# Kernel tuning notes

Measured on AMD Instinct MI355X. Metric: run time of the kernel, lower is better.

The kernel has to match this reference:

```python
import jax, jax.numpy as jnp
import numpy as np

N_NODES = 50000
N_EDGES = 800000
D_IN = 128
D_OUT = 128


def setup_inputs() -> dict:
    key = jax.random.key(0)
    k1, k2, k3, k4, k5 = jax.random.split(key, 5)
    x = jax.random.normal(k1, (N_NODES, D_IN), dtype=jnp.float32)
    # fc weight, torch Linear convention: [out_dim, in_dim]
    W = jax.random.normal(k2, (D_OUT, D_IN), dtype=jnp.float32) * (1.0 / np.sqrt(D_IN))
    # attn_fc weight: [1, 2*out_dim], no bias
    a = jax.random.normal(k3, (1, 2 * D_OUT), dtype=jnp.float32) * (1.0 / np.sqrt(2 * D_OUT))
    src = jax.random.randint(k4, (N_EDGES,), 0, N_NODES)
    dst = jax.random.randint(k5, (N_EDGES,), 0, N_NODES)
    return {"x": x, "W": W, "a": a, "src": src, "dst": dst}


def reference(x, W, a, src, dst):
    # h = fc(x)
    h = x @ W.T  # [N, D_OUT]
    # attn_fc(cat([h_src, h_dst])) == h_src @ a[:D] + h_dst @ a[D:] (linear, no bias),
    # so precompute per-node scalars instead of materializing [E, 2*D_OUT].
    a_src = a[0, :D_OUT]
    a_dst = a[0, D_OUT:]
    s = h @ a_src  # [N]
    d = h @ a_dst  # [N]
    e = jax.nn.sigmoid(s[src] + d[dst])[:, None]  # [E, 1]
    msg = e * h[src]  # [E, D_OUT]  edge gather + weight
    # reduce: f[v] = sum over incoming edges of e * h_src
    f = jax.ops.segment_sum(msg, dst, num_segments=N_NODES)  # [N, D_OUT]
    return f
```

## Files before the change

### kernel.cpp

```cpp
#include <hip/hip_runtime.h>
#include <hip/hip_bf16.h>
#include <stdint.h>

#define NN 50000
#define NE 800000
#define DD 128
#define NBKT 1563
#define BCH 4096
#define BGRID ((NE + BCH - 1) / BCH)
#define CAP 640
#define SPILL_CAP 32768
#define GROWS 64
#define GGRID ((NN + GROWS - 1) / GROWS)

typedef __attribute__((ext_vector_type(8))) unsigned short ushort8;
typedef __attribute__((ext_vector_type(8))) short short8;
typedef __attribute__((ext_vector_type(4))) float f32x4;

__device__ inline uint32_t cvtpk(float lo, float hi) {
    uint32_t r;
    asm("v_cvt_pk_bf16_f32 %0, %1, %2" : "=v"(r) : "v"(lo), "v"(hi));
    return r;
}
__device__ inline float bf_lo(uint32_t u) { return __uint_as_float(u << 16); }
__device__ inline float bf_hi(uint32_t u) { return __uint_as_float(u & 0xffff0000u); }

__global__ __launch_bounds__(256) void prep_k(const float* __restrict__ W,
                                              uint16_t* __restrict__ Wb,
                                              int* __restrict__ cntg) {
    int t = threadIdx.x;
    if (blockIdx.x == 0) {
        for (int k = t; k < NBKT + 4; k += 256) cntg[k] = 0;
    }
    int i = blockIdx.x * 256 + t;
    if (i < DD * DD) {
        uint32_t u = __float_as_uint(W[i]);
        Wb[i] = (uint16_t)((u + 0x7fffu + ((u >> 16) & 1u)) >> 16);
    }
}

__global__ __launch_bounds__(256) void fused_k(const float* __restrict__ x,
                                               const uint16_t* __restrict__ Wb,
                                               const float* __restrict__ a,
                                               const int* __restrict__ src,
                                               const int* __restrict__ dst,
                                               uint16_t* __restrict__ hb,
                                               float* __restrict__ sArr,
                                               float* __restrict__ dArr,
                                               int* __restrict__ cntg,
                                               int* __restrict__ scnt,
                                               uint32_t* __restrict__ rec,
                                               uint2* __restrict__ spill) {
    __shared__ int lh[NBKT];
    __shared__ int gb[NBKT];
    const int t = threadIdx.x;

    if ((int)blockIdx.x < GGRID) {
        const int l = t & 63, wid = t >> 6;
        const int r0 = blockIdx.x * GROWS;
        const int lr = l & 15, lk = l >> 4;

        f32x4 acc[8];
        #pragma unroll
        for (int c = 0; c < 8; ++c) acc[c] = f32x4{0.f, 0.f, 0.f, 0.f};

        const int arow = r0 + wid * 16 + lr;
        const int lrow = (arow < NN) ? arow : (NN - 1);
        const float* xp = x + (size_t)lrow * DD + lk * 8;

        #pragma unroll
        for (int kc = 0; kc < 4; ++kc) {
            float4 v0 = *(const float4*)(xp + kc * 32);
            float4 v1 = *(const float4*)(xp + kc * 32 + 4);
            union { uint32_t u[4]; short8 s; } A;
            A.u[0] = cvtpk(v0.x, v0.y); A.u[1] = cvtpk(v0.z, v0.w);
            A.u[2] = cvtpk(v1.x, v1.y); A.u[3] = cvtpk(v1.z, v1.w);
            #pragma unroll
            for (int c = 0; c < 8; ++c) {
                int col = c * 16 + lr;
                short8 bf_ = *(const short8*)(Wb + (size_t)col * DD + kc * 32 + lk * 8);
                acc[c] = __builtin_amdgcn_mfma_f32_16x16x32_bf16(A.s, bf_, acc[c], 0, 0, 0);
            }
        }

        float avs[8], avd[8];
        #pragma unroll
        for (int c = 0; c < 8; ++c) {
            avs[c] = a[c * 16 + lr];
            avd[c] = a[DD + c * 16 + lr];
        }
        #pragma unroll
        for (int i = 0; i < 4; ++i) {
            float ps = 0.f, pd = 0.f;
            #pragma unroll
            for (int c = 0; c < 8; ++c) {
                ps = fmaf(acc[c][i], avs[c], ps);
                pd = fmaf(acc[c][i], avd[c], pd);
            }
            #pragma unroll
            for (int o = 8; o > 0; o >>= 1) {
                ps += __shfl_xor(ps, o);
                pd += __shfl_xor(pd, o);
            }
            int row = r0 + wid * 16 + lk * 4 + i;
            if (lr == 0 && row < NN) { sArr[row] = ps; dArr[row] = pd; }
        }

        #pragma unroll
        for (int i = 0; i < 4; ++i) {
            int row = r0 + wid * 16 + lk * 4 + i;
            if (row < NN) {
                union { uint32_t u[4]; ushort8 s; } H;
                H.u[0] = cvtpk(acc[0][i], acc[1][i]);
                H.u[1] = cvtpk(acc[2][i], acc[3][i]);
                H.u[2] = cvtpk(acc[4][i], acc[5][i]);
                H.u[3] = cvtpk(acc[6][i], acc[7][i]);
                *(ushort8*)(hb + (size_t)row * DD + lr * 8) = H.s;
            }
        }
    } else {
        int bb = blockIdx.x - GGRID;
        for (int k = t; k < NBKT; k += 256) lh[k] = 0;
        __syncthreads();
        int base = bb * BCH;
        unsigned pk[16]; int bk[16];
        #pragma unroll
        for (int i = 0; i < 16; ++i) {
            int idx = base + i * 256 + t;
            if (idx < NE) {
                int s_ = src[idx], d_ = dst[idx];
                bk[i] = d_ >> 5;
                pk[i] = ((unsigned)(d_ & 31) << 16) | (unsigned)s_;
                atomicAdd(&lh[bk[i]], 1);
            } else bk[i] = -1;
        }
        __syncthreads();
        for (int k = t; k < NBKT; k += 256) {
            int c = lh[k];
            lh[k] = 0;
            gb[k] = c ? atomicAdd(&cntg[k], c) : 0;
        }
        __syncthreads();
        #pragma unroll
        for (int i = 0; i < 16; ++i) {
            if (bk[i] >= 0) {
                int sl = atomicAdd(&lh[bk[i]], 1);
                int p = gb[bk[i]] + sl;
                if (p < CAP) {
                    rec[(size_t)bk[i] * CAP + p] = pk[i];
                } else {
                    int sp = atomicAdd(scnt, 1);
                    if (sp < SPILL_CAP)
                        spill[sp] = make_uint2(pk[i] & 0xffffu,
                                               (unsigned)(bk[i] * 32 + (int)(pk[i] >> 16)));
                }
            }
        }
    }
}

__global__ __launch_bounds__(256) void bsort_agg_k(const uint16_t* __restrict__ hb,
                                                   const float* __restrict__ sA,
                                                   const float* __restrict__ dA,
                                                   const int* __restrict__ cntg,
                                                   const uint32_t* __restrict__ rec,
                                                   const int* __restrict__ scnt,
                                                   const uint2* __restrict__ spill,
                                                   float* __restrict__ out) {
    __shared__ uint32_t srt[CAP];
    __shared__ float    eL[CAP];
    __shared__ float dAl[32];
    __shared__ int h32[32];
    __shared__ int s33[33];
    __shared__ int curw[32];
    int t = threadIdx.x, l = t & 63, wid = t >> 6;
    int b = blockIdx.x;
    int cnt = cntg[b]; if (cnt > CAP) cnt = CAP;
    int beg = b * CAP;
    int n0 = b * 32;
    int ns = *scnt; if (ns > SPILL_CAP) ns = SPILL_CAP;
    if (t < 32) {
        h32[t] = 0;
        int n = n0 + t;
        dAl[t] = (n < NN) ? dA[n] : 0.f;
    }
    __syncthreads();

    uint32_t rc[3]; float er[3]; int nrc = 0;
    for (int j = t; j < cnt; j += 256) {
        uint32_t r = rec[beg + j];
        rc[nrc] = r;
        atomicAdd(&h32[r >> 16], 1);
        float z = sA[r & 0xffffu] + dAl[r >> 16];
        er[nrc] = 1.f / (1.f + __expf(-z));
        ++nrc;
    }
    __syncthreads();
    if (wid == 0) {
        int v = (l < 32) ? h32[l] : 0;
        int inc = v;
        #pragma unroll
        for (int o = 1; o < 32; o <<= 1) {
            int nb = __shfl_up(inc, o);
            if (l >= o) inc += nb;
        }
        if (l < 32) { s33[l + 1] = inc; curw[l] = inc - v; }
        if (l == 0) s33[0] = 0;
    }
    __syncthreads();
    for (int k = 0; k < nrc; ++k) {
        uint32_t r = rc[k];
        int p = atomicAdd(&curw[r >> 16], 1);
        srt[p] = r;
        eL[p] = er[k];
    }
    __syncthreads();

    const int q = l >> 4, sl = l & 15;
    const char* hbp = (const char*)hb;
    #pragma unroll 1
    for (int rr = 0; rr < 8; ++rr) {
        int d = wid * 8 + rr;
        int n = n0 + d;
        if (n >= NN) break;
        int js = s33[d], je = s33[d + 1];
        float acc[8] = {0.f,0.f,0.f,0.f,0.f,0.f,0.f,0.f};
        for (int j = js; j < je; j += 8) {
            int j0 = j + q, j1 = j + 4 + q;
            bool v0 = j0 < je, v1 = j1 < je;
            uint32_t r0 = srt[v0 ? j0 : js];
            uint32_t r1 = srt[v1 ? j1 : js];
            float e0 = v0 ? eL[j0] : 0.f;
            float e1 = v1 ? eL[j1] : 0.f;
            uint4 u0 = *(const uint4*)(hbp + (size_t)(r0 & 0xffffu) * 256 + sl * 16);
            uint4 u1 = *(const uint4*)(hbp + (size_t)(r1 & 0xffffu) * 256 + sl * 16);
            acc[0] = fmaf(e0, bf_lo(u0.x), acc[0]); acc[1] = fmaf(e0, bf_hi(u0.x), acc[1]);
            acc[2] = fmaf(e0, bf_lo(u0.y), acc[2]); acc[3] = fmaf(e0, bf_hi(u0.y), acc[3]);
            acc[4] = fmaf(e0, bf_lo(u0.z), acc[4]); acc[5] = fmaf(e0, bf_hi(u0.z), acc[5]);
            acc[6] = fmaf(e0, bf_lo(u0.w), acc[6]); acc[7] = fmaf(e0, bf_hi(u0.w), acc[7]);
            acc[0] = fmaf(e1, bf_lo(u1.x), acc[0]); acc[1] = fmaf(e1, bf_hi(u1.x), acc[1]);
            acc[2] = fmaf(e1, bf_lo(u1.y), acc[2]); acc[3] = fmaf(e1, bf_hi(u1.y), acc[3]);
            acc[4] = fmaf(e1, bf_lo(u1.z), acc[4]); acc[5] = fmaf(e1, bf_hi(u1.z), acc[5]);
            acc[6] = fmaf(e1, bf_lo(u1.w), acc[6]); acc[7] = fmaf(e1, bf_hi(u1.w), acc[7]);
        }
        #pragma unroll
        for (int k = 0; k < 8; ++k) {
            acc[k] += __shfl_xor(acc[k], 16);
            acc[k] += __shfl_xor(acc[k], 32);
        }
        if (ns > 0) {
            for (int i = 0; i < ns; ++i) {
                uint2 sp = spill[i];
                if ((int)sp.y == n) {
                    float z = sA[sp.x] + dAl[d];
                    float e = 1.f / (1.f + __expf(-z));
                    uint4 u = *(const uint4*)(hbp + (size_t)sp.x * 256 + sl * 16);
                    acc[0] = fmaf(e, bf_lo(u.x), acc[0]); acc[1] = fmaf(e, bf_hi(u.x), acc[1]);
                    acc[2] = fmaf(e, bf_lo(u.y), acc[2]); acc[3] = fmaf(e, bf_hi(u.y), acc[3]);
                    acc[4] = fmaf(e, bf_lo(u.z), acc[4]); acc[5] = fmaf(e, bf_hi(u.z), acc[5]);
                    acc[6] = fmaf(e, bf_lo(u.w), acc[6]); acc[7] = fmaf(e, bf_hi(u.w), acc[7]);
                }
            }
        }
        float vx = (q == 0) ? acc[0] : (q == 1) ? acc[2] : (q == 2) ? acc[4] : acc[6];
        float vy = (q == 0) ? acc[1] : (q == 1) ? acc[3] : (q == 2) ? acc[5] : acc[7];
        float* orow = out + (size_t)n * DD;
        orow[(2 * q) * 16 + sl]     = vx;
        orow[(2 * q + 1) * 16 + sl] = vy;
    }
}

__global__ __launch_bounds__(256) void edge_atomic_k(const int* __restrict__ src, const int* __restrict__ dst,
                                                     const float* __restrict__ sArr, const float* __restrict__ dArr,
                                                     const uint32_t* __restrict__ hb, float* __restrict__ out) {
    int wid = threadIdx.x >> 6, l = threadIdx.x & 63;
    int e = blockIdx.x * 4 + wid;
    if (e >= NE) return;
    int sv = src[e], dv = dst[e];
    float z = sArr[sv] + dArr[dv];
    float ev = 1.0f / (1.0f + __expf(-z));
    uint32_t u = hb[(size_t)sv * 64 + l];
    int colx = 32 * (l & 3) + (l >> 2);
    atomicAdd(&out[(size_t)dv * DD + colx],      ev * bf_lo(u));
    atomicAdd(&out[(size_t)dv * DD + colx + 16], ev * bf_hi(u));
}

extern "C" void kernel_launch(void* const* d_in, const int* in_sizes, int n_in,
                              void* d_out, int out_size, void* d_ws, size_t ws_size,
                              hipStream_t stream) {
    const float* x  = (const float*)d_in[0];
    const float* W  = (const float*)d_in[1];
    const float* a  = (const float*)d_in[2];
    const int* src  = (const int*)d_in[3];
    const int* dst  = (const int*)d_in[4];
    float* out = (float*)d_out;

    char* p = (char*)d_ws;
    uint16_t* hb = (uint16_t*)p;            p += (size_t)NN * DD * 2;
    uint16_t* Wb = (uint16_t*)p;            p += (size_t)DD * DD * 2;
    float* sA    = (float*)p;               p += (size_t)NN * 4;
    float* dA    = (float*)p;               p += (size_t)NN * 4;
    int*   cntg  = (int*)p;                 p += (size_t)NBKT * 4;
    int*   scnt  = (int*)p;                 p += 16;
    uint32_t* rec = (uint32_t*)(((uintptr_t)p + 15) & ~(uintptr_t)15);
    p = (char*)(rec + (size_t)NBKT * CAP);
    uint2* spill = (uint2*)p;               p += (size_t)SPILL_CAP * 8;
    size_t need  = (size_t)(p - (char*)d_ws);

    if (ws_size >= need) {
        prep_k<<<64, 256, 0, stream>>>(W, Wb, cntg);
        fused_k<<<GGRID + BGRID, 256, 0, stream>>>(x, Wb, a, src, dst,
                                                   hb, sA, dA, cntg, scnt, rec, spill);
        bsort_agg_k<<<NBKT, 256, 0, stream>>>(hb, sA, dA, cntg, rec, scnt, spill, out);
    } else {
        hipMemsetAsync(out, 0, sizeof(float) * (size_t)NN * DD, stream);
        prep_k<<<64, 256, 0, stream>>>(W, Wb, cntg);
        fused_k<<<GGRID, 256, 0, stream>>>(x, Wb, a, src, dst,
                                           hb, sA, dA, cntg, scnt, rec, spill);
        edge_atomic_k<<<NE / 4, 256, 0, stream>>>(src, dst, sA, dA, (const uint32_t*)hb, out);
    }
}
```

Before: 71.34 us.

## Shrink dst buckets to 16 nodes and sort edges by source segment

Halves the destination bucket size (3125 buckets of 16 nodes, CAP 384) so twice as many aggregation blocks run, with less LDS per block. Within each block, edges are binned by destination node and also by a coarse source-node segment (four ranges), and blocks start at staggered segments. The aim is better L2 locality on gathered h rows and more parallelism. Each 16-lane quarter-wave now owns one destination node and walks its edges two at a time, so the cross-quarter shuffle reduction is gone, at the cost of less memory-level parallelism per node and a higher chance of spills with the smaller CAP.

```diff
diff --git a/kernel.cpp b/kernel.cpp
--- a/kernel.cpp
+++ b/kernel.cpp
@@ -5,13 +5,14 @@
 #define NN 50000
 #define NE 800000
 #define DD 128
-#define NBKT 1563
+#define NBKT 3125
 #define BCH 4096
 #define BGRID ((NE + BCH - 1) / BCH)
-#define CAP 640
+#define CAP 384
 #define SPILL_CAP 32768
 #define GROWS 64
 #define GGRID ((NN + GROWS - 1) / GROWS)
+#define NSEG 4
 
 typedef __attribute__((ext_vector_type(8))) unsigned short ushort8;
 typedef __attribute__((ext_vector_type(8))) short short8;
@@ -29,8 +30,8 @@
                                               uint16_t* __restrict__ Wb,
                                               int* __restrict__ cntg) {
     int t = threadIdx.x;
-    if (blockIdx.x == 0) {
-        for (int k = t; k < NBKT + 4; k += 256) cntg[k] = 0;
+    if (blockIdx.x < 13) {
+        for (int k = blockIdx.x * 256 + t; k < NBKT + 4; k += 13 * 256) cntg[k] = 0;
     }
     int i = blockIdx.x * 256 + t;
     if (i < DD * DD) {
@@ -129,8 +130,8 @@
             int idx = base + i * 256 + t;
             if (idx < NE) {
                 int s_ = src[idx], d_ = dst[idx];
-                bk[i] = d_ >> 5;
-                pk[i] = ((unsigned)(d_ & 31) << 16) | (unsigned)s_;
+                bk[i] = d_ >> 4;
+                pk[i] = ((unsigned)(d_ & 15) << 16) | (unsigned)s_;
                 atomicAdd(&lh[bk[i]], 1);
             } else bk[i] = -1;
         }
@@ -152,7 +153,7 @@
                     int sp = atomicAdd(scnt, 1);
                     if (sp < SPILL_CAP)
                         spill[sp] = make_uint2(pk[i] & 0xffffu,
-                                               (unsigned)(bk[i] * 32 + (int)(pk[i] >> 16)));
+                                               (unsigned)(bk[i] * 16 + (int)(pk[i] >> 16)));
                 }
             }
         }
@@ -169,68 +170,71 @@
                                                    float* __restrict__ out) {
     __shared__ uint32_t srt[CAP];
     __shared__ float    eL[CAP];
-    __shared__ float dAl[32];
-    __shared__ int h32[32];
-    __shared__ int s33[33];
-    __shared__ int curw[32];
+    __shared__ float dAl[16];
+    __shared__ int hbin[NSEG * 16];
+    __shared__ int soff[NSEG * 16 + 1];
+    __shared__ int curw[NSEG * 16];
     int t = threadIdx.x, l = t & 63, wid = t >> 6;
     int b = blockIdx.x;
     int cnt = cntg[b]; if (cnt > CAP) cnt = CAP;
     int beg = b * CAP;
-    int n0 = b * 32;
+    int n0 = b * 16;
     int ns = *scnt; if (ns > SPILL_CAP) ns = SPILL_CAP;
-    if (t < 32) {
-        h32[t] = 0;
-        int n = n0 + t;
-        dAl[t] = (n < NN) ? dA[n] : 0.f;
-    }
+    if (t < 64) hbin[t] = 0;
+    if (t < 16) dAl[t] = dA[n0 + t];
     __syncthreads();
 
-    uint32_t rc[3]; float er[3]; int nrc = 0;
+    uint32_t rc[2]; float er[2]; int bn[2]; int nrc = 0;
     for (int j = t; j < cnt; j += 256) {
         uint32_t r = rec[beg + j];
-        rc[nrc] = r;
-        atomicAdd(&h32[r >> 16], 1);
-        float z = sA[r & 0xffffu] + dAl[r >> 16];
+        int sv = (int)(r & 0xffffu);
+        int sg = (sv >= 12500) + (sv >= 25000) + (sv >= 37500);
+        int bin = (sg << 4) | (int)(r >> 16);
+        rc[nrc] = r; bn[nrc] = bin;
+        atomicAdd(&hbin[bin], 1);
+        float z = sA[sv] + dAl[r >> 16];
         er[nrc] = 1.f / (1.f + __expf(-z));
         ++nrc;
     }
     __syncthreads();
     if (wid == 0) {
-        int v = (l < 32) ? h32[l] : 0;
+        int v = hbin[l];
         int inc = v;
         #pragma unroll
-        for (int o = 1; o < 32; o <<= 1) {
+        for (int o = 1; o < 64; o <<= 1) {
             int nb = __shfl_up(inc, o);
             if (l >= o) inc += nb;
         }
-        if (l < 32) { s33[l + 1] = inc; curw[l] = inc - v; }
-        if (l == 0) s33[0] = 0;
+        soff[l + 1] = inc;
+        if (l == 0) soff[0] = 0;
+        curw[l] = inc - v;
     }
     __syncthreads();
     for (int k = 0; k < nrc; ++k) {
-        uint32_t r = rc[k];
-        int p = atomicAdd(&curw[r >> 16], 1);
-        srt[p] = r;
+        int p = atomicAdd(&curw[bn[k]], 1);
+        srt[p] = rc[k];
         eL[p] = er[k];
     }
     __syncthreads();
 
     const int q = l >> 4, sl = l & 15;
+    const int d = wid * 4 + q;
+    const int n = n0 + d;
     const char* hbp = (const char*)hb;
-    #pragma unroll 1
-    for (int rr = 0; rr < 8; ++rr) {
-        int d = wid * 8 + rr;
-        int n = n0 + d;
-        if (n >= NN) break;
-        int js = s33[d], je = s33[d + 1];
-        float acc[8] = {0.f,0.f,0.f,0.f,0.f,0.f,0.f,0.f};
-        for (int j = js; j < je; j += 8) {
-            int j0 = j + q, j1 = j + 4 + q;
-            bool v0 = j0 < je, v1 = j1 < je;
-            uint32_t r0 = srt[v0 ? j0 : js];
-            uint32_t r1 = srt[v1 ? j1 : js];
-            float e0 = v0 ? eL[j0] : 0.f;
+    const int s0 = (blockIdx.x & 7) >> 1;
+    float acc[8] = {0.f,0.f,0.f,0.f,0.f,0.f,0.f,0.f};
+
+    #pragma unroll
+    for (int so = 0; so < NSEG; ++so) {
+        int s = (s0 + so) & (NSEG - 1);
+        int bin = (s << 4) | d;
+        int js = soff[bin], je = soff[bin + 1];
+        for (int j = js; j < je; j += 2) {
+            int j1 = j + 1;
+            bool v1 = j1 < je;
+            uint32_t r0 = srt[j];
+            uint32_t r1 = srt[v1 ? j1 : j];
+            float e0 = eL[j];
             float e1 = v1 ? eL[j1] : 0.f;
             uint4 u0 = *(const uint4*)(hbp + (size_t)(r0 & 0xffffu) * 256 + sl * 16);
             uint4 u1 = *(const uint4*)(hbp + (size_t)(r1 & 0xffffu) * 256 + sl * 16);
@@ -243,31 +247,26 @@
             acc[4] = fmaf(e1, bf_lo(u1.z), acc[4]); acc[5] = fmaf(e1, bf_hi(u1.z), acc[5]);
             acc[6] = fmaf(e1, bf_lo(u1.w), acc[6]); acc[7] = fmaf(e1, bf_hi(u1.w), acc[7]);
         }
-        #pragma unroll
-        for (int k = 0; k < 8; ++k) {
-            acc[k] += __shfl_xor(acc[k], 16);
-            acc[k] += __shfl_xor(acc[k], 32);
-        }
-        if (ns > 0) {
-            for (int i = 0; i < ns; ++i) {
-                uint2 sp = spill[i];
-                if ((int)sp.y == n) {
-                    float z = sA[sp.x] + dAl[d];
-                    float e = 1.f / (1.f + __expf(-z));
-                    uint4 u = *(const uint4*)(hbp + (size_t)sp.x * 256 + sl * 16);
-                    acc[0] = fmaf(e, bf_lo(u.x), acc[0]); acc[1] = fmaf(e, bf_hi(u.x), acc[1]);
-                    acc[2] = fmaf(e, bf_lo(u.y), acc[2]); acc[3] = fmaf(e, bf_hi(u.y), acc[3]);
-                    acc[4] = fmaf(e, bf_lo(u.z), acc[4]); acc[5] = fmaf(e, bf_hi(u.z), acc[5]);
-                    acc[6] = fmaf(e, bf_lo(u.w), acc[6]); acc[7] = fmaf(e, bf_hi(u.w), acc[7]);
-                }
-            }
-        }
-        float vx = (q == 0) ? acc[0] : (q == 1) ? acc[2] : (q == 2) ? acc[4] : acc[6];
-        float vy = (q == 0) ? acc[1] : (q == 1) ? acc[3] : (q == 2) ? acc[5] : acc[7];
-        float* orow = out + (size_t)n * DD;
-        orow[(2 * q) * 16 + sl]     = vx;
-        orow[(2 * q + 1) * 16 + sl] = vy;
-    }
+    }
+
+    if (ns > 0) {
+        for (int i = 0; i < ns; ++i) {
+            uint2 sp = spill[i];
+            if ((int)sp.y == n) {
+                float z = sA[sp.x] + dAl[d];
+                float e = 1.f / (1.f + __expf(-z));
+                uint4 u = *(const uint4*)(hbp + (size_t)sp.x * 256 + sl * 16);
+                acc[0] = fmaf(e, bf_lo(u.x), acc[0]); acc[1] = fmaf(e, bf_hi(u.x), acc[1]);
+                acc[2] = fmaf(e, bf_lo(u.y), acc[2]); acc[3] = fmaf(e, bf_hi(u.y), acc[3]);
+                acc[4] = fmaf(e, bf_lo(u.z), acc[4]); acc[5] = fmaf(e, bf_hi(u.z), acc[5]);
+                acc[6] = fmaf(e, bf_lo(u.w), acc[6]); acc[7] = fmaf(e, bf_hi(u.w), acc[7]);
+            }
+        }
+    }
+
+    float* orow = out + (size_t)n * DD;
+    #pragma unroll
+    for (int k = 0; k < 8; ++k) orow[k * 16 + sl] = acc[k];
 }
 
 __global__ __launch_bounds__(256) void edge_atomic_k(const int* __restrict__ src, const int* __restrict__ dst,
```

Measured after the change: 71.55 us. No clear change (+0.3%).
